# Kernel optimization log

Measured on AMD Instinct MI355X. Metric: run time of the kernel, lower is better.

## Reference

```python
import jax, jax.numpy as jnp
import numpy as np

H = 512                      # hidden_dim
C, T, F = 2, 128, 257        # output_dims
FLAT = C * T * F             # 65792 flattened spectrogram frame
CD, SD = 256, 256            # content_dim, style_dim
D_IN = CD + SD + FLAT        # GRU input size


def setup_inputs() -> dict:
    key = jax.random.key(0)
    ks = jax.random.split(key, 8)
    B, S = 4, 16
    sc = 0.02  # small init so tanh/sigmoid stay in a sane range
    return {
        "content_emb": jax.random.normal(ks[0], (B, S, CD), jnp.float32),
        "style_emb": jax.random.normal(ks[1], (B, SD), jnp.float32),
        "start_token": jax.random.normal(ks[2], (FLAT,), jnp.float32),
        "W_ih": jax.random.normal(ks[3], (3 * H, D_IN), jnp.float32) * sc,
        "W_hh": jax.random.normal(ks[4], (3 * H, H), jnp.float32) * sc,
        "b_ih": jnp.zeros((3 * H,), jnp.float32),
        "b_hh": jnp.zeros((3 * H,), jnp.float32),
        "W_proj": jax.random.normal(ks[5], (FLAT, H), jnp.float32) * sc,
        "b_proj": jnp.zeros((FLAT,), jnp.float32),
    }


def _gru_cell(x, h, W_ih, W_hh, b_ih, b_hh):
    # PyTorch GRU gate order: r, z, n
    gi = x @ W_ih.T + b_ih          # (B, 3H)
    gh = h @ W_hh.T + b_hh          # (B, 3H)
    i_r, i_z, i_n = jnp.split(gi, 3, axis=-1)
    h_r, h_z, h_n = jnp.split(gh, 3, axis=-1)
    r = jax.nn.sigmoid(i_r + h_r)
    z = jax.nn.sigmoid(i_z + h_z)
    n = jnp.tanh(i_n + r * h_n)
    return (1.0 - z) * n + z * h


def reference(content_emb, style_emb, start_token, W_ih, W_hh, b_ih, b_hh, W_proj, b_proj):
    B, S, _ = content_emb.shape
    h0 = jnp.zeros((B, H), content_emb.dtype)
    prev0 = jnp.broadcast_to(start_token, (B, FLAT))

    def step(carry, c_s):
        h, prev = carry
        # concat [content_s, style, prev_output] -> (B, D_IN)
        x = jnp.concatenate([c_s, style_emb, prev], axis=-1)
        h = _gru_cell(x, h, W_ih, W_hh, b_ih, b_hh)
        out = h @ W_proj.T + b_proj   # (B, FLAT)
        return (h, out), out

    _, outs = jax.lax.scan(step, (h0, prev0), jnp.swapaxes(content_emb, 0, 1))
    outs = jnp.swapaxes(outs, 0, 1)   # (B, S, FLAT)
    return outs.reshape(B, S, C, T, F)
```

## Files before the change

### kernel.cpp

```cpp
#include <hip/hip_runtime.h>
#include <hip/hip_bf16.h>
#include <math.h>

typedef __bf16 bf16x8 __attribute__((ext_vector_type(8)));
typedef float  f32x4  __attribute__((ext_vector_type(4)));

#define HDIM   512
#define FLAT   65792
#define DIN    66304
#define G3     1536
#define NSLAB  2056
#define NPAD   544
#define LPITCH 40
#define MT     128
#define KSPLIT 21
#define CHUNK  98

#define BH_BYTES  71581696ULL
#define MBUF_BYTES 3342336ULL
#define GIB_BYTES   393216ULL
#define HALL_BYTES  131072ULL
#define HBF_BYTES    65536ULL

__device__ __forceinline__ ushort f2bf(float f) {
    uint u = __float_as_uint(f);
    u += 0x7FFFu + ((u >> 16) & 1u);
    return (ushort)(u >> 16);
}

__global__ __launch_bounds__(256) void buildBh(const float* __restrict__ Wp,
                                               const float* __restrict__ bproj,
                                               const float* __restrict__ start,
                                               ushort* __restrict__ Bh) {
    __shared__ ushort tr[512 * 33];
    const int slab = blockIdx.x;
    const int tid  = threadIdx.x;
    for (int idx = tid; idx < 32 * 512; idx += 256) {
        const int k = idx >> 9;
        const int n = idx & 511;
        tr[n * 33 + k] = f2bf(Wp[(size_t)(slab * 32 + k) * 512 + n]);
    }
    __syncthreads();
    uint* out = (uint*)(Bh + (size_t)slab * 17408);
    for (int d = tid; d < 8704; d += 256) {
        const int n  = d >> 4;
        const int k2 = (d & 15) * 2;
        ushort lo, hi;
        if (n < 512)      { lo = tr[n * 33 + k2];            hi = tr[n * 33 + k2 + 1]; }
        else if (n == 512){ lo = f2bf(bproj[slab * 32 + k2]); hi = f2bf(bproj[slab * 32 + k2 + 1]); }
        else if (n == 513){ lo = f2bf(start[slab * 32 + k2]); hi = f2bf(start[slab * 32 + k2 + 1]); }
        else              { lo = 0; hi = 0; }
        out[d] = (uint)lo | ((uint)hi << 16);
    }
}

__global__ __launch_bounds__(1024) void gemmM(const float* __restrict__ Wih,
                                              const ushort* __restrict__ Bh,
                                              float* __restrict__ Mbuf) {
    __shared__ ushort Alds[MT * LPITCH];
    __shared__ ushort Blds[NPAD * LPITCH];
    const int tid  = threadIdx.x;
    const int lane = tid & 63;
    const int wave = tid >> 6;
    const int wm   = wave >> 1;
    const int wn   = wave & 1;
    const int lrow = lane & 15;
    const int quad = lane >> 4;
    const int bid   = blockIdx.x;
    const int mtile = bid % 12;
    const int kc    = bid / 12;
    const int s0 = kc * CHUNK;
    const int s1 = min(s0 + CHUNK, NSLAB);

    const int arow = tid >> 3;
    const int aseg = tid & 7;
    const float* aPtr = Wih + (size_t)(mtile * MT + arow) * DIN + 512 + aseg * 4;

    f32x4 acc[17];
#pragma unroll
    for (int t = 0; t < 17; ++t) acc[t] = (f32x4){0.f, 0.f, 0.f, 0.f};

    float4 aReg;
    uint4  bReg0 = {}, bReg1 = {}, bReg2 = {};
    {
        const size_t sb = (size_t)s0 * 17408;
        aReg  = *(const float4*)(aPtr + (size_t)s0 * 32);
        bReg0 = *(const uint4*)(Bh + sb + (size_t)tid * 8);
        bReg1 = *(const uint4*)(Bh + sb + (size_t)(tid + 1024) * 8);
        if (tid < 128) bReg2 = *(const uint4*)(Bh + sb + (size_t)(tid + 2048) * 8);
    }
    for (int s = s0; s < s1; ++s) {
        {
            uint2 ap;
            ap.x = (uint)f2bf(aReg.x) | ((uint)f2bf(aReg.y) << 16);
            ap.y = (uint)f2bf(aReg.z) | ((uint)f2bf(aReg.w) << 16);
            *(uint2*)&Alds[arow * LPITCH + aseg * 4] = ap;
            *(uint4*)&Blds[(tid >> 2) * LPITCH + (tid & 3) * 8] = bReg0;
            const int c1 = tid + 1024;
            *(uint4*)&Blds[(c1 >> 2) * LPITCH + (c1 & 3) * 8] = bReg1;
            if (tid < 128) {
                const int c2 = tid + 2048;
                *(uint4*)&Blds[(c2 >> 2) * LPITCH + (c2 & 3) * 8] = bReg2;
            }
        }
        __syncthreads();
        if (s + 1 < s1) {
            const size_t sb = (size_t)(s + 1) * 17408;
            aReg  = *(const float4*)(aPtr + (size_t)(s + 1) * 32);
            bReg0 = *(const uint4*)(Bh + sb + (size_t)tid * 8);
            bReg1 = *(const uint4*)(Bh + sb + (size_t)(tid + 1024) * 8);
            if (tid < 128) bReg2 = *(const uint4*)(Bh + sb + (size_t)(tid + 2048) * 8);
        }
        const bf16x8 af = __builtin_bit_cast(bf16x8,
            *(const uint4*)&Alds[(wm * 16 + lrow) * LPITCH + quad * 8]);
#pragma unroll
        for (int t = 0; t < 17; ++t) {
            const bf16x8 bf = __builtin_bit_cast(bf16x8,
                *(const uint4*)&Blds[(wn * 272 + t * 16 + lrow) * LPITCH + quad * 8]);
            acc[t] = __builtin_amdgcn_mfma_f32_16x16x32_bf16(af, bf, acc[t], 0, 0, 0);
        }
        __syncthreads();
    }
#pragma unroll
    for (int t = 0; t < 17; ++t) {
        const int col = wn * 272 + t * 16 + lrow;
#pragma unroll
        for (int r = 0; r < 4; ++r) {
            const int row = mtile * MT + wm * 16 + quad * 4 + r;
            atomicAdd(&Mbuf[(size_t)row * NPAD + col], acc[t][r]);
        }
    }
}

__global__ __launch_bounds__(1024) void gemmMDirect(const float* __restrict__ Wih,
                                                    const float* __restrict__ Wp,
                                                    const float* __restrict__ bproj,
                                                    const float* __restrict__ start,
                                                    float* __restrict__ Mbuf) {
    __shared__ ushort Alds[MT * LPITCH];
    __shared__ ushort Blds[NPAD * LPITCH];
    const int tid  = threadIdx.x;
    const int lane = tid & 63;
    const int wave = tid >> 6;
    const int wm   = wave >> 1;
    const int wn   = wave & 1;
    const int lrow = lane & 15;
    const int quad = lane >> 4;
    const int bid   = blockIdx.x;
    const int mtile = bid % 12;
    const int kc    = bid / 12;
    const int s0 = kc * CHUNK;
    const int s1 = min(s0 + CHUNK, NSLAB);

    const int arow = tid >> 3;
    const int aseg = tid & 7;
    const float* aPtr = Wih + (size_t)(mtile * MT + arow) * DIN + 512 + aseg * 4;

    const int bk = tid >> 5;
    const int bn0 = (tid & 31) * 4;
    const int ek = tid & 31;
    const float* esrc = (tid < 32) ? bproj : start;

    for (int idx = tid; idx < 30 * LPITCH; idx += 1024) Blds[514 * LPITCH + idx] = 0;

    f32x4 acc[17];
#pragma unroll
    for (int t = 0; t < 17; ++t) acc[t] = (f32x4){0.f, 0.f, 0.f, 0.f};

    float4 aReg;
    float4 bReg[4];
    float  eReg = 0.f;
    {
        aReg = *(const float4*)(aPtr + (size_t)s0 * 32);
        const float* bbase = Wp + (size_t)(s0 * 32 + bk) * 512 + bn0;
#pragma unroll
        for (int q = 0; q < 4; ++q) bReg[q] = *(const float4*)(bbase + q * 128);
        if (tid < 64) eReg = esrc[s0 * 32 + ek];
    }
    for (int s = s0; s < s1; ++s) {
        {
            uint2 ap;
            ap.x = (uint)f2bf(aReg.x) | ((uint)f2bf(aReg.y) << 16);
            ap.y = (uint)f2bf(aReg.z) | ((uint)f2bf(aReg.w) << 16);
            *(uint2*)&Alds[arow * LPITCH + aseg * 4] = ap;
#pragma unroll
            for (int q = 0; q < 4; ++q) {
                const int n = bn0 + q * 128;
                Blds[(n + 0) * LPITCH + bk] = f2bf(bReg[q].x);
                Blds[(n + 1) * LPITCH + bk] = f2bf(bReg[q].y);
                Blds[(n + 2) * LPITCH + bk] = f2bf(bReg[q].z);
                Blds[(n + 3) * LPITCH + bk] = f2bf(bReg[q].w);
            }
            if (tid < 64) Blds[(512 + (tid >> 5)) * LPITCH + ek] = f2bf(eReg);
        }
        __syncthreads();
        if (s + 1 < s1) {
            aReg = *(const float4*)(aPtr + (size_t)(s + 1) * 32);
            const float* bbase = Wp + (size_t)((s + 1) * 32 + bk) * 512 + bn0;
#pragma unroll
            for (int q = 0; q < 4; ++q) bReg[q] = *(const float4*)(bbase + q * 128);
            if (tid < 64) eReg = esrc[(s + 1) * 32 + ek];
        }
        const bf16x8 af = __builtin_bit_cast(bf16x8,
            *(const uint4*)&Alds[(wm * 16 + lrow) * LPITCH + quad * 8]);
#pragma unroll
        for (int t = 0; t < 17; ++t) {
            const bf16x8 bf = __builtin_bit_cast(bf16x8,
                *(const uint4*)&Blds[(wn * 272 + t * 16 + lrow) * LPITCH + quad * 8]);
            acc[t] = __builtin_amdgcn_mfma_f32_16x16x32_bf16(af, bf, acc[t], 0, 0, 0);
        }
        __syncthreads();
    }
#pragma unroll
    for (int t = 0; t < 17; ++t) {
        const int col = wn * 272 + t * 16 + lrow;
#pragma unroll
        for (int r = 0; r < 4; ++r) {
            const int row = mtile * MT + wm * 16 + quad * 4 + r;
            atomicAdd(&Mbuf[(size_t)row * NPAD + col], acc[t][r]);
        }
    }
}

__global__ __launch_bounds__(256) void giBase(const float* __restrict__ Wih,
                                              const float* __restrict__ content,
                                              const float* __restrict__ style,
                                              const float* __restrict__ bih,
                                              const float* __restrict__ Mbuf,
                                              float* __restrict__ giB) {
    const int j = (blockIdx.x * blockDim.x + threadIdx.x) >> 6;
    if (j >= G3) return;
    const int lane = threadIdx.x & 63;
    const int b = lane >> 4;
    const int s = lane & 15;
    const float* wr = Wih + (size_t)j * DIN;
    const float* cp = content + (size_t)lane * 256;
    const float* sp = style + (size_t)b * 256;
    float acc = 0.f;
#pragma unroll 4
    for (int d = 0; d < 256; d += 4) {
        const float4 w = *(const float4*)(wr + d);
        const float4 x = *(const float4*)(cp + d);
        acc += w.x * x.x + w.y * x.y + w.z * x.z + w.w * x.w;
    }
#pragma unroll 4
    for (int d = 0; d < 256; d += 4) {
        const float4 w = *(const float4*)(wr + 256 + d);
        const float4 x = *(const float4*)(sp + d);
        acc += w.x * x.x + w.y * x.y + w.z * x.z + w.w * x.w;
    }
    acc += bih[j] + ((s == 0) ? Mbuf[(size_t)j * NPAD + 513] : Mbuf[(size_t)j * NPAD + 512]);
    giB[(size_t)lane * G3 + j] = acc;
}

__global__ __launch_bounds__(256) void stepK(const float* __restrict__ Mbuf,
                                             const float* __restrict__ Whh,
                                             const float* __restrict__ bhh,
                                             const float* __restrict__ giB,
                                             float* __restrict__ hAll,
                                             ushort* __restrict__ hBf,
                                             const int s) {
    const int gw   = (blockIdx.x * blockDim.x + threadIdx.x) >> 6;
    const int lane = threadIdx.x & 63;
    const int b = gw & 3;
    const int j = gw >> 2;
    float dMr = 0.f, dMz = 0.f, dMn = 0.f, dWr = 0.f, dWz = 0.f, dWn = 0.f;
    if (s > 0) {
        const float* h = hAll + (size_t)((s - 1) * 4 + b) * HDIM;
        float hr[8];
#pragma unroll
        for (int i = 0; i < 8; ++i) hr[i] = h[i * 64 + lane];
        const float* M0 = Mbuf + (size_t)j * NPAD;
        const float* M1 = Mbuf + (size_t)(j + 512) * NPAD;
        const float* M2 = Mbuf + (size_t)(j + 1024) * NPAD;
        const float* W0 = Whh + (size_t)j * HDIM;
        const float* W1 = Whh + (size_t)(j + 512) * HDIM;
        const float* W2 = Whh + (size_t)(j + 1024) * HDIM;
#pragma unroll
        for (int i = 0; i < 8; ++i) {
            const int d = i * 64 + lane;
            dMr += M0[d] * hr[i]; dMz += M1[d] * hr[i]; dMn += M2[d] * hr[i];
            dWr += W0[d] * hr[i]; dWz += W1[d] * hr[i]; dWn += W2[d] * hr[i];
        }
#pragma unroll
        for (int m = 1; m < 64; m <<= 1) {
            dMr += __shfl_xor(dMr, m); dMz += __shfl_xor(dMz, m); dMn += __shfl_xor(dMn, m);
            dWr += __shfl_xor(dWr, m); dWz += __shfl_xor(dWz, m); dWn += __shfl_xor(dWn, m);
        }
    }
    if (lane == 0) {
        const float* gb = giB + (size_t)(b * 16 + s) * G3;
        const float gir = gb[j] + dMr;
        const float giz = gb[j + 512] + dMz;
        const float gin = gb[j + 1024] + dMn;
        const float ghr = bhh[j] + dWr;
        const float ghz = bhh[j + 512] + dWz;
        const float ghn = bhh[j + 1024] + dWn;
        const float r = 1.f / (1.f + expf(-(gir + ghr)));
        const float z = 1.f / (1.f + expf(-(giz + ghz)));
        const float n = tanhf(gin + r * ghn);
        const float hp = (s > 0) ? hAll[(size_t)((s - 1) * 4 + b) * HDIM + j] : 0.f;
        const float hn = (1.f - z) * n + z * hp;
        hAll[(size_t)(s * 4 + b) * HDIM + j] = hn;
        hBf[(size_t)(s * 4 + b) * HDIM + j] = f2bf(hn);
    }
}

__global__ __launch_bounds__(256) void projK(const float* __restrict__ Wp,
                                             const float* __restrict__ bproj,
                                             const ushort* __restrict__ hBf,
                                             float* __restrict__ out) {
    const int lane = threadIdx.x & 63;
    const int wave = threadIdx.x >> 6;
    const int f0   = blockIdx.x * 256 + wave * 64;
    const int lrow = lane & 15;
    const int quad = lane >> 4;
    f32x4 acc[4][4];
#pragma unroll
    for (int pt = 0; pt < 4; ++pt)
#pragma unroll
        for (int ft = 0; ft < 4; ++ft) acc[pt][ft] = (f32x4){0.f, 0.f, 0.f, 0.f};

    for (int d0 = 0; d0 < HDIM; d0 += 32) {
        bf16x8 afr[4];
#pragma unroll
        for (int pt = 0; pt < 4; ++pt)
            afr[pt] = __builtin_bit_cast(bf16x8,
                *(const uint4*)(hBf + (size_t)(pt * 16 + lrow) * HDIM + d0 + quad * 8));
#pragma unroll
        for (int ft = 0; ft < 4; ++ft) {
            const float* wrow = Wp + (size_t)(f0 + ft * 16 + lrow) * HDIM + d0 + quad * 8;
            const float4 w0 = *(const float4*)(wrow);
            const float4 w1 = *(const float4*)(wrow + 4);
            uint4 pr;
            pr.x = (uint)f2bf(w0.x) | ((uint)f2bf(w0.y) << 16);
            pr.y = (uint)f2bf(w0.z) | ((uint)f2bf(w0.w) << 16);
            pr.z = (uint)f2bf(w1.x) | ((uint)f2bf(w1.y) << 16);
            pr.w = (uint)f2bf(w1.z) | ((uint)f2bf(w1.w) << 16);
            const bf16x8 bfr = __builtin_bit_cast(bf16x8, pr);
#pragma unroll
            for (int pt = 0; pt < 4; ++pt)
                acc[pt][ft] = __builtin_amdgcn_mfma_f32_16x16x32_bf16(afr[pt], bfr, acc[pt][ft], 0, 0, 0);
        }
    }
#pragma unroll
    for (int pt = 0; pt < 4; ++pt)
#pragma unroll
        for (int ft = 0; ft < 4; ++ft) {
            const int f = f0 + ft * 16 + lrow;
            const float bp = bproj[f];
#pragma unroll
            for (int r = 0; r < 4; ++r) {
                const int p = pt * 16 + quad * 4 + r;
                const int ss = p >> 2;
                const int bb = p & 3;
                out[(size_t)(bb * 16 + ss) * FLAT + f] = acc[pt][ft][r] + bp;
            }
        }
}

extern "C" void kernel_launch(void* const* d_in, const int* in_sizes, int n_in,
                              void* d_out, int out_size, void* d_ws, size_t ws_size,
                              hipStream_t stream) {
    const float* content = (const float*)d_in[0];
    const float* style   = (const float*)d_in[1];
    const float* start   = (const float*)d_in[2];
    const float* Wih     = (const float*)d_in[3];
    const float* Whh     = (const float*)d_in[4];
    const float* bih     = (const float*)d_in[5];
    const float* bhh     = (const float*)d_in[6];
    const float* Wproj   = (const float*)d_in[7];
    const float* bproj   = (const float*)d_in[8];
    float* out = (float*)d_out;

    const size_t needFast = BH_BYTES + MBUF_BYTES + GIB_BYTES + HALL_BYTES + HBF_BYTES;
    const bool fast = (ws_size >= needFast);

    char* ws = (char*)d_ws;
    const size_t base = fast ? BH_BYTES : 0;
    ushort* Bh   = (ushort*)ws;
    float*  Mbuf = (float*)(ws + base);
    float*  giB  = (float*)(ws + base + MBUF_BYTES);
    float*  hAll = (float*)(ws + base + MBUF_BYTES + GIB_BYTES);
    ushort* hBf  = (ushort*)(ws + base + MBUF_BYTES + GIB_BYTES + HALL_BYTES);

    hipMemsetAsync(Mbuf, 0, MBUF_BYTES, stream);
    if (fast) {
        buildBh<<<NSLAB, 256, 0, stream>>>(Wproj, bproj, start, Bh);
        gemmM<<<12 * KSPLIT, 1024, 0, stream>>>(Wih, Bh, Mbuf);
    } else {
        gemmMDirect<<<12 * KSPLIT, 1024, 0, stream>>>(Wih, Wproj, bproj, start, Mbuf);
    }
    giBase<<<384, 256, 0, stream>>>(Wih, content, style, bih, Mbuf, giB);
    for (int s = 0; s < 16; ++s)
        stepK<<<512, 256, 0, stream>>>(Mbuf, Whh, bhh, giB, hAll, hBf, s);
    projK<<<FLAT / 256, 256, 0, stream>>>(Wproj, bproj, hBf, out);
}
```

Measured before the change: 936.6 us.

## Pre-swizzle W_proj into MFMA fragment layout and drop LDS staging in gemmM

```diff
diff --git a/kernel.cpp b/kernel.cpp
--- a/kernel.cpp
+++ b/kernel.cpp
@@ -10,214 +10,159 @@
 #define DIN    66304
 #define G3     1536
 #define NSLAB  2056
-#define NPAD   544
-#define LPITCH 40
-#define MT     128
+#define MS     512
 #define KSPLIT 21
 #define CHUNK  98
 
-#define BH_BYTES  71581696ULL
-#define MBUF_BYTES 3342336ULL
-#define GIB_BYTES   393216ULL
-#define HALL_BYTES  131072ULL
-#define HBF_BYTES    65536ULL
+#define BH_BYTES   67371008ULL
+#define MBUF_BYTES  3145728ULL
+#define BP_BYTES       6144ULL
+#define ST_BYTES       6144ULL
+#define GIB_BYTES    393216ULL
+#define HALL_BYTES   131072ULL
+#define HBF_BYTES     65536ULL
 
 __device__ __forceinline__ ushort f2bf(float f) {
     uint u = __float_as_uint(f);
     u += 0x7FFFu + ((u >> 16) & 1u);
     return (ushort)(u >> 16);
 }
+__device__ __forceinline__ uint pk2(float a, float b) {
+    return (uint)f2bf(a) | ((uint)f2bf(b) << 16);
+}
 
 __global__ __launch_bounds__(256) void buildBh(const float* __restrict__ Wp,
-                                               const float* __restrict__ bproj,
-                                               const float* __restrict__ start,
                                                ushort* __restrict__ Bh) {
-    __shared__ ushort tr[512 * 33];
-    const int slab = blockIdx.x;
-    const int tid  = threadIdx.x;
-    for (int idx = tid; idx < 32 * 512; idx += 256) {
-        const int k = idx >> 9;
-        const int n = idx & 511;
-        tr[n * 33 + k] = f2bf(Wp[(size_t)(slab * 32 + k) * 512 + n]);
-    }
-    __syncthreads();
-    uint* out = (uint*)(Bh + (size_t)slab * 17408);
-    for (int d = tid; d < 8704; d += 256) {
-        const int n  = d >> 4;
-        const int k2 = (d & 15) * 2;
-        ushort lo, hi;
-        if (n < 512)      { lo = tr[n * 33 + k2];            hi = tr[n * 33 + k2 + 1]; }
-        else if (n == 512){ lo = f2bf(bproj[slab * 32 + k2]); hi = f2bf(bproj[slab * 32 + k2 + 1]); }
-        else if (n == 513){ lo = f2bf(start[slab * 32 + k2]); hi = f2bf(start[slab * 32 + k2 + 1]); }
-        else              { lo = 0; hi = 0; }
-        out[d] = (uint)lo | ((uint)hi << 16);
-    }
-}
-
-__global__ __launch_bounds__(1024) void gemmM(const float* __restrict__ Wih,
-                                              const ushort* __restrict__ Bh,
-                                              float* __restrict__ Mbuf) {
-    __shared__ ushort Alds[MT * LPITCH];
-    __shared__ ushort Blds[NPAD * LPITCH];
+    const int s    = blockIdx.x;
+    const int lane = threadIdx.x & 63;
+    const int wave = threadIdx.x >> 6;
+    const int lrow = lane & 15;
+    const int quad = lane >> 4;
+    const float* base = Wp + (size_t)s * 32 * 512;
+    ushort* out = Bh + (size_t)s * 16384;
+#pragma unroll
+    for (int i = 0; i < 8; ++i) {
+        const int t = wave + i * 4;
+        const int col = t * 16 + lrow;
+        float v[8];
+#pragma unroll
+        for (int j = 0; j < 8; ++j)
+            v[j] = base[(size_t)(quad * 8 + j) * 512 + col];
+        uint4 pr;
+        pr.x = pk2(v[0], v[1]);
+        pr.y = pk2(v[2], v[3]);
+        pr.z = pk2(v[4], v[5]);
+        pr.w = pk2(v[6], v[7]);
+        *(uint4*)(out + (size_t)t * 512 + (size_t)lane * 8) = pr;
+    }
+}
+
+__global__ __launch_bounds__(512, 2) void gemmM(const float* __restrict__ Wih,
+                                                const ushort* __restrict__ Bh,
+                                                const float* __restrict__ bproj,
+                                                const float* __restrict__ start,
+                                                float* __restrict__ Mbuf,
+                                                float* __restrict__ bpA,
+                                                float* __restrict__ stA) {
     const int tid  = threadIdx.x;
     const int lane = tid & 63;
     const int wave = tid >> 6;
-    const int wm   = wave >> 1;
-    const int wn   = wave & 1;
+    const int mg   = wave >> 2;
+    const int ng   = wave & 3;
     const int lrow = lane & 15;
     const int quad = lane >> 4;
-    const int bid   = blockIdx.x;
-    const int mtile = bid % 12;
-    const int kc    = bid / 12;
+    const int mtile = blockIdx.x % 12;
+    const int kc    = blockIdx.x / 12;
     const int s0 = kc * CHUNK;
     const int s1 = min(s0 + CHUNK, NSLAB);
 
-    const int arow = tid >> 3;
-    const int aseg = tid & 7;
-    const float* aPtr = Wih + (size_t)(mtile * MT + arow) * DIN + 512 + aseg * 4;
-
-    f32x4 acc[17];
-#pragma unroll
-    for (int t = 0; t < 17; ++t) acc[t] = (f32x4){0.f, 0.f, 0.f, 0.f};
-
-    float4 aReg;
-    uint4  bReg0 = {}, bReg1 = {}, bReg2 = {};
-    {
-        const size_t sb = (size_t)s0 * 17408;
-        aReg  = *(const float4*)(aPtr + (size_t)s0 * 32);
-        bReg0 = *(const uint4*)(Bh + sb + (size_t)tid * 8);
-        bReg1 = *(const uint4*)(Bh + sb + (size_t)(tid + 1024) * 8);
-        if (tid < 128) bReg2 = *(const uint4*)(Bh + sb + (size_t)(tid + 2048) * 8);
-    }
+    const int rowBase = mtile * 128 + mg * 64 + lrow;
+    const float* aP[4];
+#pragma unroll
+    for (int mf = 0; mf < 4; ++mf)
+        aP[mf] = Wih + (size_t)(rowBase + mf * 16) * DIN + 512 + quad * 8;
+    const ushort* bBase = Bh + (size_t)(ng * 8) * 512 + (size_t)lane * 8;
+
+    f32x4 acc[4][8];
+#pragma unroll
+    for (int mf = 0; mf < 4; ++mf)
+#pragma unroll
+        for (int nf = 0; nf < 8; ++nf) acc[mf][nf] = (f32x4){0.f, 0.f, 0.f, 0.f};
+    float bpAcc[4] = {0.f, 0.f, 0.f, 0.f};
+    float stAcc[4] = {0.f, 0.f, 0.f, 0.f};
+
+    float4 a0[4], a1[4];
+#pragma unroll
+    for (int mf = 0; mf < 4; ++mf) {
+        a0[mf] = *(const float4*)(aP[mf] + (size_t)s0 * 32);
+        a1[mf] = *(const float4*)(aP[mf] + (size_t)s0 * 32 + 4);
+    }
+
     for (int s = s0; s < s1; ++s) {
-        {
-            uint2 ap;
-            ap.x = (uint)f2bf(aReg.x) | ((uint)f2bf(aReg.y) << 16);
-            ap.y = (uint)f2bf(aReg.z) | ((uint)f2bf(aReg.w) << 16);
-            *(uint2*)&Alds[arow * LPITCH + aseg * 4] = ap;
-            *(uint4*)&Blds[(tid >> 2) * LPITCH + (tid & 3) * 8] = bReg0;
-            const int c1 = tid + 1024;
-            *(uint4*)&Blds[(c1 >> 2) * LPITCH + (c1 & 3) * 8] = bReg1;
-            if (tid < 128) {
-                const int c2 = tid + 2048;
-                *(uint4*)&Blds[(c2 >> 2) * LPITCH + (c2 & 3) * 8] = bReg2;
-            }
-        }
-        __syncthreads();
+        uint4 bReg[8];
+        const ushort* bs = bBase + (size_t)s * 16384;
+#pragma unroll
+        for (int nf = 0; nf < 8; ++nf)
+            bReg[nf] = *(const uint4*)(bs + nf * 512);
+        if (ng == 0) {
+            const float4 bp0 = *(const float4*)(bproj + s * 32 + quad * 8);
+            const float4 bp1 = *(const float4*)(bproj + s * 32 + quad * 8 + 4);
+            const float4 st0 = *(const float4*)(start + s * 32 + quad * 8);
+            const float4 st1 = *(const float4*)(start + s * 32 + quad * 8 + 4);
+#pragma unroll
+            for (int mf = 0; mf < 4; ++mf) {
+                bpAcc[mf] += a0[mf].x * bp0.x + a0[mf].y * bp0.y + a0[mf].z * bp0.z + a0[mf].w * bp0.w
+                           + a1[mf].x * bp1.x + a1[mf].y * bp1.y + a1[mf].z * bp1.z + a1[mf].w * bp1.w;
+                stAcc[mf] += a0[mf].x * st0.x + a0[mf].y * st0.y + a0[mf].z * st0.z + a0[mf].w * st0.w
+                           + a1[mf].x * st1.x + a1[mf].y * st1.y + a1[mf].z * st1.z + a1[mf].w * st1.w;
+            }
+        }
+        bf16x8 af[4];
+#pragma unroll
+        for (int mf = 0; mf < 4; ++mf) {
+            uint4 pr;
+            pr.x = pk2(a0[mf].x, a0[mf].y);
+            pr.y = pk2(a0[mf].z, a0[mf].w);
+            pr.z = pk2(a1[mf].x, a1[mf].y);
+            pr.w = pk2(a1[mf].z, a1[mf].w);
+            af[mf] = __builtin_bit_cast(bf16x8, pr);
+        }
         if (s + 1 < s1) {
-            const size_t sb = (size_t)(s + 1) * 17408;
-            aReg  = *(const float4*)(aPtr + (size_t)(s + 1) * 32);
-            bReg0 = *(const uint4*)(Bh + sb + (size_t)tid * 8);
-            bReg1 = *(const uint4*)(Bh + sb + (size_t)(tid + 1024) * 8);
-            if (tid < 128) bReg2 = *(const uint4*)(Bh + sb + (size_t)(tid + 2048) * 8);
-        }
-        const bf16x8 af = __builtin_bit_cast(bf16x8,
-            *(const uint4*)&Alds[(wm * 16 + lrow) * LPITCH + quad * 8]);
-#pragma unroll
-        for (int t = 0; t < 17; ++t) {
-            const bf16x8 bf = __builtin_bit_cast(bf16x8,
-                *(const uint4*)&Blds[(wn * 272 + t * 16 + lrow) * LPITCH + quad * 8]);
-            acc[t] = __builtin_amdgcn_mfma_f32_16x16x32_bf16(af, bf, acc[t], 0, 0, 0);
-        }
-        __syncthreads();
-    }
-#pragma unroll
-    for (int t = 0; t < 17; ++t) {
-        const int col = wn * 272 + t * 16 + lrow;
-#pragma unroll
-        for (int r = 0; r < 4; ++r) {
-            const int row = mtile * MT + wm * 16 + quad * 4 + r;
-            atomicAdd(&Mbuf[(size_t)row * NPAD + col], acc[t][r]);
-        }
-    }
-}
-
-__global__ __launch_bounds__(1024) void gemmMDirect(const float* __restrict__ Wih,
-                                                    const float* __restrict__ Wp,
-                                                    const float* __restrict__ bproj,
-                                                    const float* __restrict__ start,
-                                                    float* __restrict__ Mbuf) {
-    __shared__ ushort Alds[MT * LPITCH];
-    __shared__ ushort Blds[NPAD * LPITCH];
-    const int tid  = threadIdx.x;
-    const int lane = tid & 63;
-    const int wave = tid >> 6;
-    const int wm   = wave >> 1;
-    const int wn   = wave & 1;
-    const int lrow = lane & 15;
-    const int quad = lane >> 4;
-    const int bid   = blockIdx.x;
-    const int mtile = bid % 12;
-    const int kc    = bid / 12;
-    const int s0 = kc * CHUNK;
-    const int s1 = min(s0 + CHUNK, NSLAB);
-
-    const int arow = tid >> 3;
-    const int aseg = tid & 7;
-    const float* aPtr = Wih + (size_t)(mtile * MT + arow) * DIN + 512 + aseg * 4;
-
-    const int bk = tid >> 5;
-    const int bn0 = (tid & 31) * 4;
-    const int ek = tid & 31;
-    const float* esrc = (tid < 32) ? bproj : start;
-
-    for (int idx = tid; idx < 30 * LPITCH; idx += 1024) Blds[514 * LPITCH + idx] = 0;
-
-    f32x4 acc[17];
-#pragma unroll
-    for (int t = 0; t < 17; ++t) acc[t] = (f32x4){0.f, 0.f, 0.f, 0.f};
-
-    float4 aReg;
-    float4 bReg[4];
-    float  eReg = 0.f;
-    {
-        aReg = *(const float4*)(aPtr + (size_t)s0 * 32);
-        const float* bbase = Wp + (size_t)(s0 * 32 + bk) * 512 + bn0;
-#pragma unroll
-        for (int q = 0; q < 4; ++q) bReg[q] = *(const float4*)(bbase + q * 128);
-        if (tid < 64) eReg = esrc[s0 * 32 + ek];
-    }
-    for (int s = s0; s < s1; ++s) {
-        {
-            uint2 ap;
-            ap.x = (uint)f2bf(aReg.x) | ((uint)f2bf(aReg.y) << 16);
-            ap.y = (uint)f2bf(aReg.z) | ((uint)f2bf(aReg.w) << 16);
-            *(uint2*)&Alds[arow * LPITCH + aseg * 4] = ap;
-#pragma unroll
-            for (int q = 0; q < 4; ++q) {
-                const int n = bn0 + q * 128;
-                Blds[(n + 0) * LPITCH + bk] = f2bf(bReg[q].x);
-                Blds[(n + 1) * LPITCH + bk] = f2bf(bReg[q].y);
-                Blds[(n + 2) * LPITCH + bk] = f2bf(bReg[q].z);
-                Blds[(n + 3) * LPITCH + bk] = f2bf(bReg[q].w);
-            }
-            if (tid < 64) Blds[(512 + (tid >> 5)) * LPITCH + ek] = f2bf(eReg);
-        }
-        __syncthreads();
-        if (s + 1 < s1) {
-            aReg = *(const float4*)(aPtr + (size_t)(s + 1) * 32);
-            const float* bbase = Wp + (size_t)((s + 1) * 32 + bk) * 512 + bn0;
-#pragma unroll
-            for (int q = 0; q < 4; ++q) bReg[q] = *(const float4*)(bbase + q * 128);
-            if (tid < 64) eReg = esrc[(s + 1) * 32 + ek];
-        }
-        const bf16x8 af = __builtin_bit_cast(bf16x8,
-            *(const uint4*)&Alds[(wm * 16 + lrow) * LPITCH + quad * 8]);
-#pragma unroll
-        for (int t = 0; t < 17; ++t) {
-            const bf16x8 bf = __builtin_bit_cast(bf16x8,
-                *(const uint4*)&Blds[(wn * 272 + t * 16 + lrow) * LPITCH + quad * 8]);
-            acc[t] = __builtin_amdgcn_mfma_f32_16x16x32_bf16(af, bf, acc[t], 0, 0, 0);
-        }
-        __syncthreads();
-    }
-#pragma unroll
-    for (int t = 0; t < 17; ++t) {
-        const int col = wn * 272 + t * 16 + lrow;
-#pragma unroll
-        for (int r = 0; r < 4; ++r) {
-            const int row = mtile * MT + wm * 16 + quad * 4 + r;
-            atomicAdd(&Mbuf[(size_t)row * NPAD + col], acc[t][r]);
+#pragma unroll
+            for (int mf = 0; mf < 4; ++mf) {
+                a0[mf] = *(const float4*)(aP[mf] + (size_t)(s + 1) * 32);
+                a1[mf] = *(const float4*)(aP[mf] + (size_t)(s + 1) * 32 + 4);
+            }
+        }
+#pragma unroll
+        for (int nf = 0; nf < 8; ++nf) {
+            const bf16x8 bf = __builtin_bit_cast(bf16x8, bReg[nf]);
+#pragma unroll
+            for (int mf = 0; mf < 4; ++mf)
+                acc[mf][nf] = __builtin_amdgcn_mfma_f32_16x16x32_bf16(af[mf], bf, acc[mf][nf], 0, 0, 0);
+        }
+    }
+#pragma unroll
+    for (int mf = 0; mf < 4; ++mf)
+#pragma unroll
+        for (int nf = 0; nf < 8; ++nf) {
+            const int col = (ng * 8 + nf) * 16 + lrow;
+#pragma unroll
+            for (int r = 0; r < 4; ++r) {
+                const int row = mtile * 128 + mg * 64 + mf * 16 + quad * 4 + r;
+                atomicAdd(&Mbuf[(size_t)row * MS + col], acc[mf][nf][r]);
+            }
+        }
+    if (ng == 0) {
+#pragma unroll
+        for (int mf = 0; mf < 4; ++mf) {
+            float bp = bpAcc[mf], st = stAcc[mf];
+            bp += __shfl_xor(bp, 16); bp += __shfl_xor(bp, 32);
+            st += __shfl_xor(st, 16); st += __shfl_xor(st, 32);
+            if (lane < 16) {
+                atomicAdd(&bpA[rowBase + mf * 16], bp);
+                atomicAdd(&stA[rowBase + mf * 16], st);
+            }
         }
     }
 }
@@ -226,7 +171,8 @@
                                               const float* __restrict__ content,
                                               const float* __restrict__ style,
                                               const float* __restrict__ bih,
-                                              const float* __restrict__ Mbuf,
+                                              const float* __restrict__ bpA,
+                                              const float* __restrict__ stA,
                                               float* __restrict__ giB) {
     const int j = (blockIdx.x * blockDim.x + threadIdx.x) >> 6;
     if (j >= G3) return;
@@ -249,7 +195,7 @@
         const float4 x = *(const float4*)(sp + d);
         acc += w.x * x.x + w.y * x.y + w.z * x.z + w.w * x.w;
     }
-    acc += bih[j] + ((s == 0) ? Mbuf[(size_t)j * NPAD + 513] : Mbuf[(size_t)j * NPAD + 512]);
+    acc += bih[j] + ((s == 0) ? stA[j] : bpA[j]);
     giB[(size_t)lane * G3 + j] = acc;
 }
 
@@ -270,9 +216,9 @@
         float hr[8];
 #pragma unroll
         for (int i = 0; i < 8; ++i) hr[i] = h[i * 64 + lane];
-        const float* M0 = Mbuf + (size_t)j * NPAD;
-        const float* M1 = Mbuf + (size_t)(j + 512) * NPAD;
-        const float* M2 = Mbuf + (size_t)(j + 1024) * NPAD;
+        const float* M0 = Mbuf + (size_t)j * MS;
+        const float* M1 = Mbuf + (size_t)(j + 512) * MS;
+        const float* M2 = Mbuf + (size_t)(j + 1024) * MS;
         const float* W0 = Whh + (size_t)j * HDIM;
         const float* W1 = Whh + (size_t)(j + 512) * HDIM;
         const float* W2 = Whh + (size_t)(j + 1024) * HDIM;
@@ -333,10 +279,10 @@
             const float4 w0 = *(const float4*)(wrow);
             const float4 w1 = *(const float4*)(wrow + 4);
             uint4 pr;
-            pr.x = (uint)f2bf(w0.x) | ((uint)f2bf(w0.y) << 16);
-            pr.y = (uint)f2bf(w0.z) | ((uint)f2bf(w0.w) << 16);
-            pr.z = (uint)f2bf(w1.x) | ((uint)f2bf(w1.y) << 16);
-            pr.w = (uint)f2bf(w1.z) | ((uint)f2bf(w1.w) << 16);
+            pr.x = pk2(w0.x, w0.y);
+            pr.y = pk2(w0.z, w0.w);
+            pr.z = pk2(w1.x, w1.y);
+            pr.w = pk2(w1.z, w1.w);
             const bf16x8 bfr = __builtin_bit_cast(bf16x8, pr);
 #pragma unroll
             for (int pt = 0; pt < 4; ++pt)
@@ -373,25 +319,19 @@
     const float* bproj   = (const float*)d_in[8];
     float* out = (float*)d_out;
 
-    const size_t needFast = BH_BYTES + MBUF_BYTES + GIB_BYTES + HALL_BYTES + HBF_BYTES;
-    const bool fast = (ws_size >= needFast);
-
     char* ws = (char*)d_ws;
-    const size_t base = fast ? BH_BYTES : 0;
-    ushort* Bh   = (ushort*)ws;
-    float*  Mbuf = (float*)(ws + base);
-    float*  giB  = (float*)(ws + base + MBUF_BYTES);
-    float*  hAll = (float*)(ws + base + MBUF_BYTES + GIB_BYTES);
-    ushort* hBf  = (ushort*)(ws + base + MBUF_BYTES + GIB_BYTES + HALL_BYTES);
-
-    hipMemsetAsync(Mbuf, 0, MBUF_BYTES, stream);
-    if (fast) {
-        buildBh<<<NSLAB, 256, 0, stream>>>(Wproj, bproj, start, Bh);
-        gemmM<<<12 * KSPLIT, 1024, 0, stream>>>(Wih, Bh, Mbuf);
-    } else {
-        gemmMDirect<<<12 * KSPLIT, 1024, 0, stream>>>(Wih, Wproj, bproj, start, Mbuf);
-    }
-    giBase<<<384, 256, 0, stream>>>(Wih, content, style, bih, Mbuf, giB);
+    ushort* Bh   = (ushort*)(ws);
+    float*  Mbuf = (float*)(ws + BH_BYTES);
+    float*  bpA  = (float*)(ws + BH_BYTES + MBUF_BYTES);
+    float*  stA  = (float*)(ws + BH_BYTES + MBUF_BYTES + BP_BYTES);
+    float*  giB  = (float*)(ws + BH_BYTES + MBUF_BYTES + BP_BYTES + ST_BYTES);
+    float*  hAll = (float*)(ws + BH_BYTES + MBUF_BYTES + BP_BYTES + ST_BYTES + GIB_BYTES);
+    ushort* hBf  = (ushort*)(ws + BH_BYTES + MBUF_BYTES + BP_BYTES + ST_BYTES + GIB_BYTES + HALL_BYTES);
+
+    hipMemsetAsync(Mbuf, 0, MBUF_BYTES + BP_BYTES + ST_BYTES, stream);
+    buildBh<<<NSLAB, 256, 0, stream>>>(Wproj, Bh);
+    gemmM<<<12 * KSPLIT, 512, 0, stream>>>(Wih, Bh, bproj, start, Mbuf, bpA, stA);
+    giBase<<<384, 256, 0, stream>>>(Wih, content, style, bih, bpA, stA, giB);
     for (int s = 0; s < 16; ++s)
         stepK<<<512, 256, 0, stream>>>(Mbuf, Whh, bhh, giB, hAll, hBf, s);
     projK<<<FLAT / 256, 256, 0, stream>>>(Wproj, bproj, hBf, out);
```

Measured after the change: 1.030 ms. 1.1x slower.
